# Performance work log

Hardware: AMD Instinct MI355X
Metric: run time of the kernel (lower is better)

## Reference

```python
import jax, jax.numpy as jnp
import numpy as np


def log_g(x):
    # log of g(x) = x+0.5 for x>=0, sigmoid(x) for x<0, computed stably
    return jnp.where(x >= 0, jnp.log(jax.nn.relu(x) + 0.5), -jax.nn.softplus(-x))


def setup_inputs() -> dict:
    key = jax.random.key(0)
    k1, k2 = jax.random.split(key)
    B, S, D = 4, 4096, 1024
    x = jax.random.normal(k1, (B, S, D), dtype=jnp.float32)
    W = jax.random.normal(k2, (D, 3 * D), dtype=jnp.float32) * (1.0 / np.sqrt(D))
    return {"x": x, "W": W}


def reference(x, W):
    # fused gate projection: [B,S,D] @ [D,3D] -> f_gate, i_gate, hidden
    gates = jnp.einsum('bsd,de->bse', x, W)
    f_gate, i_gate, hidden = jnp.split(gates, 3, axis=-1)

    # log-space normalized gates: log_f = log(sig(f)/(sig(f)+sig(i))) etc.
    diff = jax.nn.softplus(-f_gate) - jax.nn.softplus(-i_gate)
    log_f = -jax.nn.softplus(diff)
    log_i = -jax.nn.softplus(-diff)
    log_tilde_h = log_g(hidden)

    log_values = log_i + log_tilde_h
    # parallel scan in log space over seq axis (axis=1)
    a_star = jnp.cumsum(log_f, axis=1)
    log_h0_plus_b_star = jax.lax.cumlogsumexp(log_values - a_star, axis=1)
    h = jnp.exp(a_star + log_h0_plus_b_star)  # [B,S,D]
    return h  # to_out is Identity for expansion_factor == 1.0
```

## Files before the change

### kernel.cpp

```cpp
#include <hip/hip_runtime.h>
#include <hip/hip_fp16.h>
#include <cstdint>

typedef _Float16 half8  __attribute__((ext_vector_type(8)));
typedef _Float16 half4v __attribute__((ext_vector_type(4)));
typedef float    floatx4 __attribute__((ext_vector_type(4)));

constexpr int Bb = 4, Ss = 4096, Dd = 1024;
constexpr int Mdim = Bb * Ss;
constexpr int Ndim = 3 * Dd;
constexpr int Kdim = Dd;
constexpr int CH = 256, LCH = Ss / CH;

__device__ __forceinline__ void gload_lds16(const void* g, void* l) {
  __builtin_amdgcn_global_load_lds(
      (const __attribute__((address_space(1))) uint32_t*)g,
      (__attribute__((address_space(3))) uint32_t*)l, 16, 0, 0);
}

__device__ __forceinline__ void gate_fv(float fg, float ig, float hg,
                                        float& fw, float& v) {
  float ef = __expf(fminf(-fg, 40.f));
  float ei = __expf(fminf(-ig, 40.f));
  float r  = __builtin_amdgcn_rcpf(2.f + ef + ei);
  fw = (1.f + ei) * r;
  float iw = (1.f + ef) * r;
  float g  = hg >= 0.f ? hg + 0.5f
                       : __builtin_amdgcn_rcpf(1.f + __expf(fminf(-hg, 40.f)));
  v = iw * g;
}

__global__ __launch_bounds__(256) void cvt_k(const float* __restrict__ X,
                                             _Float16* __restrict__ X16,
                                             const float* __restrict__ W,
                                             _Float16* __restrict__ WT) {
  __shared__ float tile[32][33];
  int bid = blockIdx.x;
  if (bid < 2048) {
    const int n4 = Mdim * Kdim / 4;
    for (int i = bid * 256 + threadIdx.x; i < n4; i += 2048 * 256) {
      float4 v = ((const float4*)X)[i];
      half4v o = {(_Float16)v.x, (_Float16)v.y, (_Float16)v.z, (_Float16)v.w};
      ((half4v*)X16)[i] = o;
    }
  } else {
    int b2 = bid - 2048;
    int tx = threadIdx.x & 31, ty = threadIdx.x >> 5;
    int n0 = (b2 % 96) * 32, k0 = (b2 / 96) * 32;
#pragma unroll
    for (int j = 0; j < 4; ++j) {
      int k = ty + j * 8;
      tile[k][tx] = W[(int64_t)(k0 + k) * Ndim + n0 + tx];
    }
    __syncthreads();
#pragma unroll
    for (int j = 0; j < 4; ++j) {
      int nl = ty + j * 8;
      WT[(int64_t)(n0 + nl) * Kdim + k0 + tx] = (_Float16)tile[tx][nl];
    }
  }
}

constexpr int GBM = 256, GBN = 256, GBK = 64;
constexpr int NT = Kdim / GBK;

__global__ __launch_bounds__(512, 2) void gemm8_k(const _Float16* __restrict__ A,
                                                  const _Float16* __restrict__ BT,
                                                  _Float16* __restrict__ Cg) {
  extern __shared__ char lds[];
  const int tid = threadIdx.x;
  const int wid = tid >> 6, lane = tid & 63;
  const int wm = wid >> 2, wn = wid & 3;
  const int l15 = lane & 15, lq = lane >> 4;

  int wg = blockIdx.x;
  wg = (wg & 7) * 96 + (wg >> 3);
  const int n0 = (wg % 12) * GBN;
  const int m0 = (wg / 12) * GBM;

  int aO[4], bO[2];
#pragma unroll
  for (int mi = 0; mi < 4; ++mi) {
    int r = wm * 64 + mi * 16 + l15;
    aO[mi] = r * 128 + ((lq ^ (r & 7)) << 4);
  }
#pragma unroll
  for (int ni = 0; ni < 2; ++ni) {
    int r = wn * 32 + ni * 16 + l15;
    bO[ni] = r * 128 + ((lq ^ (r & 7)) << 4);
  }

  const int srr = (wid << 3) + (lane >> 3);
  const int ss = lane & 7;
  const _Float16* Abase = A + (size_t)m0 * Kdim;
  const _Float16* Bbase = BT + (size_t)n0 * Kdim;

  auto stage = [&](const _Float16* gsrc, int ldsHalfBase) {
#pragma unroll
    for (int round = 0; round < 2; ++round) {
      int r = (round << 6) + srr;
      int c = ss ^ (r & 7);
      gload_lds16(gsrc + (size_t)r * Kdim + (c << 3),
                  lds + ldsHalfBase + (round << 13) + (wid << 10));
    }
  };

  floatx4 acc[8][4] = {};

  stage(Abase, 0);
  stage(Bbase, 32768);
  stage(Bbase + 128 * Kdim, 49152);
  stage(Abase + 128 * Kdim, 16384);
  stage(Abase + 64, 65536);
  stage(Bbase + 64, 65536 + 32768);
  asm volatile("s_waitcnt vmcnt(4)" ::: "memory");
  __builtin_amdgcn_s_barrier();

  for (int kt = 0; kt < NT; ++kt) {
    const int cur = (kt & 1) << 16, nxt = ((kt + 1) & 1) << 16;
    const _Float16* Akt1 = Abase + (kt + 1) * GBK;
    const _Float16* Bkt1 = Bbase + (kt + 1) * GBK;
    const _Float16* Akt2 = Abase + (kt + 2) * GBK;
    const _Float16* Bkt2 = Bbase + (kt + 2) * GBK;

    half8 a[4][2], b0[2][2], b1[2][2];

#pragma unroll
    for (int mi = 0; mi < 4; ++mi)
#pragma unroll
      for (int ks = 0; ks < 2; ++ks)
        a[mi][ks] = *(const half8*)(lds + cur + (aO[mi] ^ (ks << 6)));
#pragma unroll
    for (int ni = 0; ni < 2; ++ni)
#pragma unroll
      for (int ks = 0; ks < 2; ++ks) {
        b0[ni][ks] = *(const half8*)(lds + cur + 32768 + (bO[ni] ^ (ks << 6)));
        b1[ni][ks] = *(const half8*)(lds + cur + 49152 + (bO[ni] ^ (ks << 6)));
      }
    if (kt + 1 < NT) stage(Bkt1 + 128 * Kdim, nxt + 49152);

    __builtin_amdgcn_s_setprio(1);
#pragma unroll
    for (int ks = 0; ks < 2; ++ks)
#pragma unroll
      for (int mi = 0; mi < 4; ++mi)
#pragma unroll
        for (int ni = 0; ni < 2; ++ni)
          acc[mi][ni] = __builtin_amdgcn_mfma_f32_16x16x32_f16(
              a[mi][ks], b0[ni][ks], acc[mi][ni], 0, 0, 0);
    __builtin_amdgcn_s_setprio(0);
    if (kt + 1 < NT) stage(Akt1 + 128 * Kdim, nxt + 16384);

    __builtin_amdgcn_s_barrier();
    if (kt + 2 < NT) {
      stage(Akt2, cur + 0);
      stage(Bkt2, cur + 32768);
    }

    __builtin_amdgcn_s_setprio(1);
#pragma unroll
    for (int ks = 0; ks < 2; ++ks)
#pragma unroll
      for (int mi = 0; mi < 4; ++mi)
#pragma unroll
        for (int ni = 0; ni < 2; ++ni)
          acc[mi][2 + ni] = __builtin_amdgcn_mfma_f32_16x16x32_f16(
              a[mi][ks], b1[ni][ks], acc[mi][2 + ni], 0, 0, 0);
    __builtin_amdgcn_s_setprio(0);

#pragma unroll
    for (int mi = 0; mi < 4; ++mi)
#pragma unroll
      for (int ks = 0; ks < 2; ++ks)
        a[mi][ks] = *(const half8*)(lds + cur + 16384 + (aO[mi] ^ (ks << 6)));

    __builtin_amdgcn_s_setprio(1);
#pragma unroll
    for (int ks = 0; ks < 2; ++ks)
#pragma unroll
      for (int mi = 0; mi < 4; ++mi)
#pragma unroll
        for (int ni = 0; ni < 2; ++ni)
          acc[4 + mi][ni] = __builtin_amdgcn_mfma_f32_16x16x32_f16(
              a[mi][ks], b0[ni][ks], acc[4 + mi][ni], 0, 0, 0);
#pragma unroll
    for (int ks = 0; ks < 2; ++ks)
#pragma unroll
      for (int mi = 0; mi < 4; ++mi)
#pragma unroll
        for (int ni = 0; ni < 2; ++ni)
          acc[4 + mi][2 + ni] = __builtin_amdgcn_mfma_f32_16x16x32_f16(
              a[mi][ks], b1[ni][ks], acc[4 + mi][2 + ni], 0, 0, 0);
    __builtin_amdgcn_s_setprio(0);

    if (kt < NT - 2) {
      asm volatile("s_waitcnt vmcnt(4)" ::: "memory");
      __builtin_amdgcn_s_barrier();
    } else if (kt == NT - 2) {
      asm volatile("s_waitcnt vmcnt(0)" ::: "memory");
      __builtin_amdgcn_s_barrier();
    }
  }

#pragma unroll
  for (int mf = 0; mf < 8; ++mf) {
    int row = m0 + ((mf >> 2) << 7) + wm * 64 + ((mf & 3) << 4) + (lq << 2);
#pragma unroll
    for (int nf = 0; nf < 4; ++nf) {
      int col = n0 + ((nf >> 1) << 7) + wn * 32 + ((nf & 1) << 4) + l15;
#pragma unroll
      for (int r = 0; r < 4; ++r)
        Cg[(size_t)(row + r) * Ndim + col] = (_Float16)acc[mf][nf][r];
    }
  }
}

__global__ __launch_bounds__(256) void scan1_k(const _Float16* __restrict__ G,
                                               float* __restrict__ Fc,
                                               float* __restrict__ Hc) {
  int d = threadIdx.x * 4;
  int c = blockIdx.y, b = blockIdx.z;
  const _Float16* g = G + (int64_t)(b * Ss + c * LCH) * Ndim + d;
  float h[4] = {0.f, 0.f, 0.f, 0.f};
  float F[4] = {1.f, 1.f, 1.f, 1.f};
#pragma unroll 4
  for (int s = 0; s < LCH; ++s) {
    half4v fg = *(const half4v*)(g);
    half4v ig = *(const half4v*)(g + Dd);
    half4v hg = *(const half4v*)(g + 2 * Dd);
#pragma unroll
    for (int j = 0; j < 4; ++j) {
      float fw, v;
      gate_fv((float)fg[j], (float)ig[j], (float)hg[j], fw, v);
      h[j] = fmaf(fw, h[j], v);
      F[j] *= fw;
    }
    g += Ndim;
  }
  int co = (b * CH + c) * Dd + d;
  *(floatx4*)(Fc + co) = *(floatx4*)F;
  *(floatx4*)(Hc + co) = *(floatx4*)h;
}

__global__ __launch_bounds__(256) void scan2_k(const float* __restrict__ Fc,
                                               const float* __restrict__ Hc,
                                               float* __restrict__ Carry) {
  int idx = blockIdx.x * 256 + threadIdx.x;
  int b = idx >> 10, d = idx & (Dd - 1);
  float carry = 0.f;
#pragma unroll 8
  for (int c = 0; c < CH; ++c) {
    int co = (b * CH + c) * Dd + d;
    Carry[co] = carry;
    carry = fmaf(Fc[co], carry, Hc[co]);
  }
}

__global__ __launch_bounds__(256) void scan3_k(const _Float16* __restrict__ G,
                                               const float* __restrict__ Carry,
                                               float* __restrict__ Out) {
  int d = threadIdx.x * 4;
  int c = blockIdx.y, b = blockIdx.z;
  int64_t row0 = (int64_t)(b * Ss + c * LCH);
  const _Float16* g = G + row0 * Ndim + d;
  float* o = Out + row0 * Dd + d;
  int co = (b * CH + c) * Dd + d;
  floatx4 hv = *(const floatx4*)(Carry + co);
  float h[4] = {hv[0], hv[1], hv[2], hv[3]};
#pragma unroll 4
  for (int s = 0; s < LCH; ++s) {
    half4v fg = *(const half4v*)(g);
    half4v ig = *(const half4v*)(g + Dd);
    half4v hg = *(const half4v*)(g + 2 * Dd);
#pragma unroll
    for (int j = 0; j < 4; ++j) {
      float fw, v;
      gate_fv((float)fg[j], (float)ig[j], (float)hg[j], fw, v);
      h[j] = fmaf(fw, h[j], v);
    }
    *(floatx4*)o = *(floatx4*)h;
    g += Ndim;
    o += Dd;
  }
}

extern "C" void kernel_launch(void* const* d_in, const int* in_sizes, int n_in,
                              void* d_out, int out_size, void* d_ws, size_t ws_size,
                              hipStream_t stream) {
  const float* x = (const float*)d_in[0];
  const float* W = (const float*)d_in[1];
  float* out = (float*)d_out;

  char* ws = (char*)d_ws;
  size_t off = 0;
  auto alloc = [&](size_t bytes) {
    char* p = ws + off;
    off += (bytes + 255) & ~size_t(255);
    return p;
  };
  _Float16* gates  = (_Float16*)alloc((size_t)Mdim * Ndim * 2);
  float* Fc        = (float*)alloc((size_t)Bb * CH * Dd * 4);
  float* Hc        = (float*)alloc((size_t)Bb * CH * Dd * 4);
  float* Carry     = (float*)alloc((size_t)Bb * CH * Dd * 4);
  _Float16* x16    = (_Float16*)alloc((size_t)Mdim * Kdim * 2);
  _Float16* w16t   = (_Float16*)alloc((size_t)Ndim * Kdim * 2);
  if (off > ws_size) return;

  cvt_k<<<5120, 256, 0, stream>>>(x, x16, W, w16t);
  gemm8_k<<<dim3((Mdim / GBM) * (Ndim / GBN)), 512, 131072, stream>>>(x16, w16t, gates);
  scan1_k<<<dim3(1, CH, Bb), 256, 0, stream>>>(gates, Fc, Hc);
  scan2_k<<<(Bb * Dd) / 256, 256, 0, stream>>>(Fc, Hc, Carry);
  scan3_k<<<dim3(1, CH, Bb), 256, 0, stream>>>(gates, Carry, out);
}
```

Before: 192.9 us.

## Fuse gate activation into GEMM epilogue via interleaved weight column layout

Weight columns are permuted so that each 192-wide N tile holds matching 64-column slices of the f, i and hidden gates. The GEMM epilogue can then compute the normalized forget weight and value per element and write a compact fp16 (fw, v) pair instead of three raw gate values. This cuts the GEMM output write and the scan read traffic from three halves to two per element, and removes the duplicated transcendental math from both scan passes. The cost is a smaller N tile (192 instead of 256), which lowers MMA reuse per A load and adds epilogue arithmetic inside the GEMM. Storing fw and v in fp16 instead of the raw gates may also shift numerical accuracy.

```diff
diff --git a/kernel.cpp b/kernel.cpp
--- a/kernel.cpp
+++ b/kernel.cpp
@@ -4,6 +4,7 @@
 
 typedef _Float16 half8  __attribute__((ext_vector_type(8)));
 typedef _Float16 half4v __attribute__((ext_vector_type(4)));
+typedef _Float16 half2v __attribute__((ext_vector_type(2)));
 typedef float    floatx4 __attribute__((ext_vector_type(4)));
 
 constexpr int Bb = 4, Ss = 4096, Dd = 1024;
@@ -56,17 +57,21 @@
 #pragma unroll
     for (int j = 0; j < 4; ++j) {
       int nl = ty + j * 8;
-      WT[(int64_t)(n0 + nl) * Kdim + k0 + tx] = (_Float16)tile[tx][nl];
-    }
-  }
-}
-
-constexpr int GBM = 256, GBN = 256, GBK = 64;
+      int n = n0 + nl;
+      int g = n >> 10, d = n & 1023;
+      int p = (d >> 6) * 192 + g * 64 + (d & 63);
+      WT[(int64_t)p * Kdim + k0 + tx] = (_Float16)tile[tx][nl];
+    }
+  }
+}
+
+constexpr int GBM = 256, GBN = 192, GBK = 64;
 constexpr int NT = Kdim / GBK;
+constexpr int LBUF = 57344;
 
 __global__ __launch_bounds__(512, 2) void gemm8_k(const _Float16* __restrict__ A,
                                                   const _Float16* __restrict__ BT,
-                                                  _Float16* __restrict__ Cg) {
+                                                  _Float16* __restrict__ fv) {
   extern __shared__ char lds[];
   const int tid = threadIdx.x;
   const int wid = tid >> 6, lane = tid & 63;
@@ -74,56 +79,52 @@
   const int l15 = lane & 15, lq = lane >> 4;
 
   int wg = blockIdx.x;
-  wg = (wg & 7) * 96 + (wg >> 3);
-  const int n0 = (wg % 12) * GBN;
-  const int m0 = (wg / 12) * GBM;
-
-  int aO[4], bO[2];
+  wg = (wg & 7) * 128 + (wg >> 3);
+  const int m0 = (wg >> 4) * GBM;
+  const int d0 = (wg & 15) * 64;
+
+  int aO[4];
 #pragma unroll
   for (int mi = 0; mi < 4; ++mi) {
     int r = wm * 64 + mi * 16 + l15;
     aO[mi] = r * 128 + ((lq ^ (r & 7)) << 4);
   }
-#pragma unroll
-  for (int ni = 0; ni < 2; ++ni) {
-    int r = wn * 32 + ni * 16 + l15;
-    bO[ni] = r * 128 + ((lq ^ (r & 7)) << 4);
-  }
+  const int rB = wn * 16 + l15;
+  const int bO = rB * 128 + ((lq ^ (rB & 7)) << 4);
 
   const int srr = (wid << 3) + (lane >> 3);
   const int ss = lane & 7;
   const _Float16* Abase = A + (size_t)m0 * Kdim;
-  const _Float16* Bbase = BT + (size_t)n0 * Kdim;
-
-  auto stage = [&](const _Float16* gsrc, int ldsHalfBase) {
-#pragma unroll
-    for (int round = 0; round < 2; ++round) {
+  const _Float16* Bbase = BT + (size_t)(wg & 15) * 192 * Kdim;
+
+  auto stage = [&](const _Float16* gsrc, int ldsBase, int nr) {
+#pragma unroll
+    for (int round = 0; round < 3; ++round) {
+      if (round >= nr) break;
       int r = (round << 6) + srr;
       int c = ss ^ (r & 7);
       gload_lds16(gsrc + (size_t)r * Kdim + (c << 3),
-                  lds + ldsHalfBase + (round << 13) + (wid << 10));
+                  lds + ldsBase + (round << 13) + (wid << 10));
     }
   };
 
-  floatx4 acc[8][4] = {};
-
-  stage(Abase, 0);
-  stage(Bbase, 32768);
-  stage(Bbase + 128 * Kdim, 49152);
-  stage(Abase + 128 * Kdim, 16384);
-  stage(Abase + 64, 65536);
-  stage(Bbase + 64, 65536 + 32768);
-  asm volatile("s_waitcnt vmcnt(4)" ::: "memory");
+  floatx4 acc[8][3] = {};
+
+  stage(Abase, 0, 2);
+  stage(Bbase, 32768, 3);
+  stage(Abase + 128 * Kdim, 16384, 2);
+  stage(Abase + 64, LBUF, 2);
+  stage(Bbase + 64, LBUF + 32768, 3);
+  asm volatile("s_waitcnt vmcnt(5)" ::: "memory");
   __builtin_amdgcn_s_barrier();
 
   for (int kt = 0; kt < NT; ++kt) {
-    const int cur = (kt & 1) << 16, nxt = ((kt + 1) & 1) << 16;
+    const int cur = (kt & 1) * LBUF, nxt = ((kt + 1) & 1) * LBUF;
     const _Float16* Akt1 = Abase + (kt + 1) * GBK;
-    const _Float16* Bkt1 = Bbase + (kt + 1) * GBK;
     const _Float16* Akt2 = Abase + (kt + 2) * GBK;
     const _Float16* Bkt2 = Bbase + (kt + 2) * GBK;
 
-    half8 a[4][2], b0[2][2], b1[2][2];
+    half8 a[4][2], b[3][2];
 
 #pragma unroll
     for (int mi = 0; mi < 4; ++mi)
@@ -131,13 +132,11 @@
       for (int ks = 0; ks < 2; ++ks)
         a[mi][ks] = *(const half8*)(lds + cur + (aO[mi] ^ (ks << 6)));
 #pragma unroll
-    for (int ni = 0; ni < 2; ++ni)
-#pragma unroll
-      for (int ks = 0; ks < 2; ++ks) {
-        b0[ni][ks] = *(const half8*)(lds + cur + 32768 + (bO[ni] ^ (ks << 6)));
-        b1[ni][ks] = *(const half8*)(lds + cur + 49152 + (bO[ni] ^ (ks << 6)));
-      }
-    if (kt + 1 < NT) stage(Bkt1 + 128 * Kdim, nxt + 49152);
+    for (int g = 0; g < 3; ++g)
+#pragma unroll
+      for (int ks = 0; ks < 2; ++ks)
+        b[g][ks] = *(const half8*)(lds + cur + 32768 + (g << 13) + (bO ^ (ks << 6)));
+    if (kt + 1 < NT) stage(Akt1 + 128 * Kdim, nxt + 16384, 2);
 
     __builtin_amdgcn_s_setprio(1);
 #pragma unroll
@@ -145,34 +144,22 @@
 #pragma unroll
       for (int mi = 0; mi < 4; ++mi)
 #pragma unroll
-        for (int ni = 0; ni < 2; ++ni)
-          acc[mi][ni] = __builtin_amdgcn_mfma_f32_16x16x32_f16(
-              a[mi][ks], b0[ni][ks], acc[mi][ni], 0, 0, 0);
+        for (int g = 0; g < 3; ++g)
+          acc[mi][g] = __builtin_amdgcn_mfma_f32_16x16x32_f16(
+              a[mi][ks], b[g][ks], acc[mi][g], 0, 0, 0);
     __builtin_amdgcn_s_setprio(0);
-    if (kt + 1 < NT) stage(Akt1 + 128 * Kdim, nxt + 16384);
 
     __builtin_amdgcn_s_barrier();
-    if (kt + 2 < NT) {
-      stage(Akt2, cur + 0);
-      stage(Bkt2, cur + 32768);
-    }
-
-    __builtin_amdgcn_s_setprio(1);
-#pragma unroll
-    for (int ks = 0; ks < 2; ++ks)
-#pragma unroll
-      for (int mi = 0; mi < 4; ++mi)
-#pragma unroll
-        for (int ni = 0; ni < 2; ++ni)
-          acc[mi][2 + ni] = __builtin_amdgcn_mfma_f32_16x16x32_f16(
-              a[mi][ks], b1[ni][ks], acc[mi][2 + ni], 0, 0, 0);
-    __builtin_amdgcn_s_setprio(0);
 
 #pragma unroll
     for (int mi = 0; mi < 4; ++mi)
 #pragma unroll
       for (int ks = 0; ks < 2; ++ks)
         a[mi][ks] = *(const half8*)(lds + cur + 16384 + (aO[mi] ^ (ks << 6)));
+    if (kt + 2 < NT) {
+      stage(Akt2, cur, 2);
+      stage(Bkt2, cur + 32768, 3);
+    }
 
     __builtin_amdgcn_s_setprio(1);
 #pragma unroll
@@ -180,21 +167,13 @@
 #pragma unroll
       for (int mi = 0; mi < 4; ++mi)
 #pragma unroll
-        for (int ni = 0; ni < 2; ++ni)
-          acc[4 + mi][ni] = __builtin_amdgcn_mfma_f32_16x16x32_f16(
-              a[mi][ks], b0[ni][ks], acc[4 + mi][ni], 0, 0, 0);
-#pragma unroll
-    for (int ks = 0; ks < 2; ++ks)
-#pragma unroll
-      for (int mi = 0; mi < 4; ++mi)
-#pragma unroll
-        for (int ni = 0; ni < 2; ++ni)
-          acc[4 + mi][2 + ni] = __builtin_amdgcn_mfma_f32_16x16x32_f16(
-              a[mi][ks], b1[ni][ks], acc[4 + mi][2 + ni], 0, 0, 0);
+        for (int g = 0; g < 3; ++g)
+          acc[4 + mi][g] = __builtin_amdgcn_mfma_f32_16x16x32_f16(
+              a[mi][ks], b[g][ks], acc[4 + mi][g], 0, 0, 0);
     __builtin_amdgcn_s_setprio(0);
 
     if (kt < NT - 2) {
-      asm volatile("s_waitcnt vmcnt(4)" ::: "memory");
+      asm volatile("s_waitcnt vmcnt(5)" ::: "memory");
       __builtin_amdgcn_s_barrier();
     } else if (kt == NT - 2) {
       asm volatile("s_waitcnt vmcnt(0)" ::: "memory");
@@ -202,40 +181,41 @@
     }
   }
 
-#pragma unroll
-  for (int mf = 0; mf < 8; ++mf) {
-    int row = m0 + ((mf >> 2) << 7) + wm * 64 + ((mf & 3) << 4) + (lq << 2);
-#pragma unroll
-    for (int nf = 0; nf < 4; ++nf) {
-      int col = n0 + ((nf >> 1) << 7) + wn * 32 + ((nf & 1) << 4) + l15;
-#pragma unroll
-      for (int r = 0; r < 4; ++r)
-        Cg[(size_t)(row + r) * Ndim + col] = (_Float16)acc[mf][nf][r];
-    }
-  }
-}
-
-__global__ __launch_bounds__(256) void scan1_k(const _Float16* __restrict__ G,
+  const int dcol = d0 + wn * 16 + l15;
+#pragma unroll
+  for (int hf = 0; hf < 2; ++hf)
+#pragma unroll
+    for (int mf = 0; mf < 4; ++mf) {
+      int row = m0 + hf * 128 + wm * 64 + mf * 16 + (lq << 2);
+#pragma unroll
+      for (int r = 0; r < 4; ++r) {
+        float fw, v;
+        gate_fv(acc[hf * 4 + mf][0][r], acc[hf * 4 + mf][1][r],
+                acc[hf * 4 + mf][2][r], fw, v);
+        half2v o = {(_Float16)fw, (_Float16)v};
+        *(half2v*)(fv + ((size_t)(row + r) * Dd + dcol) * 2) = o;
+      }
+    }
+}
+
+__global__ __launch_bounds__(256) void scan1_k(const _Float16* __restrict__ fv,
                                                float* __restrict__ Fc,
                                                float* __restrict__ Hc) {
   int d = threadIdx.x * 4;
   int c = blockIdx.y, b = blockIdx.z;
-  const _Float16* g = G + (int64_t)(b * Ss + c * LCH) * Ndim + d;
+  const _Float16* p = fv + ((int64_t)(b * Ss + c * LCH) * Dd + d) * 2;
   float h[4] = {0.f, 0.f, 0.f, 0.f};
   float F[4] = {1.f, 1.f, 1.f, 1.f};
 #pragma unroll 4
   for (int s = 0; s < LCH; ++s) {
-    half4v fg = *(const half4v*)(g);
-    half4v ig = *(const half4v*)(g + Dd);
-    half4v hg = *(const half4v*)(g + 2 * Dd);
+    half8 q = *(const half8*)p;
 #pragma unroll
     for (int j = 0; j < 4; ++j) {
-      float fw, v;
-      gate_fv((float)fg[j], (float)ig[j], (float)hg[j], fw, v);
-      h[j] = fmaf(fw, h[j], v);
-      F[j] *= fw;
-    }
-    g += Ndim;
+      float fr = (float)q[2 * j], vr = (float)q[2 * j + 1];
+      h[j] = fmaf(fr, h[j], vr);
+      F[j] *= fr;
+    }
+    p += Dd * 2;
   }
   int co = (b * CH + c) * Dd + d;
   *(floatx4*)(Fc + co) = *(floatx4*)F;
@@ -256,30 +236,25 @@
   }
 }
 
-__global__ __launch_bounds__(256) void scan3_k(const _Float16* __restrict__ G,
+__global__ __launch_bounds__(256) void scan3_k(const _Float16* __restrict__ fv,
                                                const float* __restrict__ Carry,
                                                float* __restrict__ Out) {
   int d = threadIdx.x * 4;
   int c = blockIdx.y, b = blockIdx.z;
-  int64_t row0 = (int64_t)(b * Ss + c * LCH);
-  const _Float16* g = G + row0 * Ndim + d;
-  float* o = Out + row0 * Dd + d;
+  int64_t m0 = (int64_t)(b * Ss + c * LCH);
+  const _Float16* p = fv + (m0 * Dd + d) * 2;
+  float* o = Out + m0 * Dd + d;
   int co = (b * CH + c) * Dd + d;
   floatx4 hv = *(const floatx4*)(Carry + co);
   float h[4] = {hv[0], hv[1], hv[2], hv[3]};
 #pragma unroll 4
   for (int s = 0; s < LCH; ++s) {
-    half4v fg = *(const half4v*)(g);
-    half4v ig = *(const half4v*)(g + Dd);
-    half4v hg = *(const half4v*)(g + 2 * Dd);
-#pragma unroll
-    for (int j = 0; j < 4; ++j) {
-      float fw, v;
-      gate_fv((float)fg[j], (float)ig[j], (float)hg[j], fw, v);
-      h[j] = fmaf(fw, h[j], v);
-    }
+    half8 q = *(const half8*)p;
+#pragma unroll
+    for (int j = 0; j < 4; ++j)
+      h[j] = fmaf((float)q[2 * j], h[j], (float)q[2 * j + 1]);
     *(floatx4*)o = *(floatx4*)h;
-    g += Ndim;
+    p += Dd * 2;
     o += Dd;
   }
 }
@@ -298,7 +273,7 @@
     off += (bytes + 255) & ~size_t(255);
     return p;
   };
-  _Float16* gates  = (_Float16*)alloc((size_t)Mdim * Ndim * 2);
+  _Float16* fv     = (_Float16*)alloc((size_t)Mdim * Dd * 2 * 2);
   float* Fc        = (float*)alloc((size_t)Bb * CH * Dd * 4);
   float* Hc        = (float*)alloc((size_t)Bb * CH * Dd * 4);
   float* Carry     = (float*)alloc((size_t)Bb * CH * Dd * 4);
@@ -307,8 +282,8 @@
   if (off > ws_size) return;
 
   cvt_k<<<5120, 256, 0, stream>>>(x, x16, W, w16t);
-  gemm8_k<<<dim3((Mdim / GBM) * (Ndim / GBN)), 512, 131072, stream>>>(x16, w16t, gates);
-  scan1_k<<<dim3(1, CH, Bb), 256, 0, stream>>>(gates, Fc, Hc);
+  gemm8_k<<<dim3((Mdim / GBM) * (Dd / 64)), 512, 114688, stream>>>(x16, w16t, fv);
+  scan1_k<<<dim3(1, CH, Bb), 256, 0, stream>>>(fv, Fc, Hc);
   scan2_k<<<(Bb * Dd) / 256, 256, 0, stream>>>(Fc, Hc, Carry);
-  scan3_k<<<dim3(1, CH, Bb), 256, 0, stream>>>(gates, Carry, out);
-}
+  scan3_k<<<dim3(1, CH, Bb), 256, 0, stream>>>(fv, Carry, out);
+}
```

After: 183.3 us. 5.0% less time.
